# Kernel optimization log

Hardware: AMD Instinct MI355X
Metric: run time of the kernel (lower is better)

The kernel has to match this reference:

```python
import jax, jax.numpy as jnp
import numpy as np

EMBED = 1024
HEADS = 16
HEAD_DIM = EMBED // HEADS


def setup_inputs() -> dict:
    key = jax.random.key(0)
    ks = jax.random.split(key, 8)
    N, S = 4, 2048
    values = jax.random.normal(ks[0], (N, S, EMBED), dtype=jnp.float32)
    keys = jax.random.normal(ks[1], (N, S, EMBED), dtype=jnp.float32)
    query = jax.random.normal(ks[2], (N, S, EMBED), dtype=jnp.float32)
    mask = jnp.ones((N, 1, 1, S), dtype=jnp.int32)
    sd = 1.0 / np.sqrt(HEAD_DIM)
    Wv = jax.random.uniform(ks[3], (HEAD_DIM, HEAD_DIM), jnp.float32, -sd, sd)
    Wk = jax.random.uniform(ks[4], (HEAD_DIM, HEAD_DIM), jnp.float32, -sd, sd)
    Wq = jax.random.uniform(ks[5], (HEAD_DIM, HEAD_DIM), jnp.float32, -sd, sd)
    so = 1.0 / np.sqrt(EMBED)
    Wo = jax.random.uniform(ks[6], (EMBED, EMBED), jnp.float32, -so, so)
    bo = jax.random.uniform(ks[7], (EMBED,), jnp.float32, -so, so)
    return {"values": values, "keys": keys, "query": query, "mask": mask,
            "Wv": Wv, "Wk": Wk, "Wq": Wq, "Wo": Wo, "bo": bo}


def reference(values, keys, query, mask, Wv, Wk, Wq, Wo, bo):
    N, Sq, _ = query.shape
    # split heads: (N, L, H, D)
    v = values.reshape(N, -1, HEADS, HEAD_DIM)
    k = keys.reshape(N, -1, HEADS, HEAD_DIM)
    q = query.reshape(N, Sq, HEADS, HEAD_DIM)
    # per-head linear projections (torch Linear: x @ W.T)
    v = jnp.einsum('nlhd,ed->nlhe', v, Wv)
    k = jnp.einsum('nlhd,ed->nlhe', k, Wk)
    q = jnp.einsum('nqhd,ed->nqhe', q, Wq)
    # energy: (N, H, Q, K)
    energy = jnp.einsum('nqhd,nkhd->nhqk', q, k)
    energy = jnp.where(mask == 0, jnp.float32(-1e20), energy)
    # NOTE: original scales by sqrt(embed_size), not sqrt(head_dim)
    attention = jax.nn.softmax(energy / jnp.sqrt(jnp.float32(EMBED)), axis=3)
    out = jnp.einsum('nhql,nlhd->nqhd', attention, v).reshape(N, Sq, EMBED)
    return out @ Wo.T + bo
```

## Files before the change

### kernel.cpp

```cpp
#include <hip/hip_runtime.h>
#include <hip/hip_bf16.h>

typedef __bf16 bf16x8 __attribute__((ext_vector_type(8)));
typedef __bf16 bf16x4 __attribute__((ext_vector_type(4)));
typedef __bf16 bf16x2 __attribute__((ext_vector_type(2)));
typedef float  f32x4  __attribute__((ext_vector_type(4)));
typedef float  f32x16 __attribute__((ext_vector_type(16)));
typedef unsigned int u32;
typedef u32 u32x4 __attribute__((ext_vector_type(4)));

#define S_  2048
#define E_  1024
#define NH_ 64

__device__ __forceinline__ f32x4 mfma16(bf16x8 a, bf16x8 b, f32x4 c) {
    return __builtin_amdgcn_mfma_f32_16x16x32_bf16(a, b, c, 0, 0, 0);
}
__device__ __forceinline__ f32x16 mfma32(bf16x8 a, bf16x8 b, f32x16 c) {
    return __builtin_amdgcn_mfma_f32_32x32x16_bf16(a, b, c, 0, 0, 0);
}
__device__ __forceinline__ u32 pack2(float a, float b) {
    bf16x2 t; t[0] = (__bf16)a; t[1] = (__bf16)b;
    return __builtin_bit_cast(u32, t);
}
__device__ __forceinline__ void swap32(u32& a, u32& b) {
    asm("v_permlane32_swap_b32 %0, %1" : "+v"(a), "+v"(b));
}
__device__ __forceinline__ f32x16 zero16() {
    f32x16 z;
#pragma unroll
    for (int i = 0; i < 16; ++i) z[i] = 0.f;
    return z;
}
__device__ __forceinline__ void gload_lds16(const void* g, void* l) {
    __builtin_amdgcn_global_load_lds(
        (const __attribute__((address_space(1))) unsigned int*)g,
        (__attribute__((address_space(3))) unsigned int*)l, 16, 0, 0);
}

__global__ __launch_bounds__(256) void k_cast_wo(const float* __restrict__ Wo,
                                                 __bf16* __restrict__ Wob) {
    int i = (blockIdx.x * 256 + threadIdx.x) * 8;
    int o = i >> 10, e0 = i & 1023;
    float4 a = *(const float4*)(Wo + i);
    float4 b = *(const float4*)(Wo + i + 4);
    bf16x8 f;
    f[0] = (__bf16)a.x; f[1] = (__bf16)a.y; f[2] = (__bf16)a.z; f[3] = (__bf16)a.w;
    f[4] = (__bf16)b.x; f[5] = (__bf16)b.y; f[6] = (__bf16)b.z; f[7] = (__bf16)b.w;
    int e_swz = (e0 & ~63) | ((e0 & 63) ^ ((o & 7) << 3));
    *(bf16x8*)(Wob + (size_t)o * 1024 + e_swz) = f;
}

__global__ __launch_bounds__(256) void k_proj(const float* __restrict__ vin,
                                              const float* __restrict__ kin,
                                              const float* __restrict__ qin,
                                              const float* __restrict__ Wv,
                                              const float* __restrict__ Wk,
                                              const float* __restrict__ Wq,
                                              __bf16* __restrict__ Qws,
                                              __bf16* __restrict__ Kws,
                                              __bf16* __restrict__ Vt) {
    const int z = blockIdx.z;
    const float* in = (z == 0) ? vin : ((z == 1) ? kin : qin);
    const float* W  = (z == 0) ? Wv  : ((z == 1) ? Wk  : Wq);
    const float scale = (z == 2) ? 0.04508422f : 1.0f;
    const int bid  = blockIdx.x;
    const int nh   = bid >> 5;
    const int sblk = (bid & 31) << 6;
    const int n = nh >> 4, h = nh & 15;
    const int lane = threadIdx.x & 63, wid = threadIdx.x >> 6;
    const int l16 = lane & 15, g = lane >> 4;

    bf16x8 Bf[4][2];
#pragma unroll
    for (int nt = 0; nt < 4; ++nt)
#pragma unroll
        for (int ks = 0; ks < 2; ++ks) {
            const float* wp = W + (nt * 16 + l16) * 64 + ks * 32 + g * 8;
            float4 a = *(const float4*)wp;
            float4 b = *(const float4*)(wp + 4);
            bf16x8 f;
            f[0] = (__bf16)(a.x * scale); f[1] = (__bf16)(a.y * scale);
            f[2] = (__bf16)(a.z * scale); f[3] = (__bf16)(a.w * scale);
            f[4] = (__bf16)(b.x * scale); f[5] = (__bf16)(b.y * scale);
            f[6] = (__bf16)(b.z * scale); f[7] = (__bf16)(b.w * scale);
            Bf[nt][ks] = f;
        }

    const int s = sblk + wid * 16 + l16;
    const float* ip = in + ((size_t)n * S_ + s) * E_ + h * 64 + g * 8;
    bf16x8 Af[2];
#pragma unroll
    for (int ks = 0; ks < 2; ++ks) {
        float4 a = *(const float4*)(ip + ks * 32);
        float4 b = *(const float4*)(ip + ks * 32 + 4);
        bf16x8 f;
        f[0] = (__bf16)a.x; f[1] = (__bf16)a.y; f[2] = (__bf16)a.z; f[3] = (__bf16)a.w;
        f[4] = (__bf16)b.x; f[5] = (__bf16)b.y; f[6] = (__bf16)b.z; f[7] = (__bf16)b.w;
        Af[ks] = f;
    }

    f32x4 acc[4];
#pragma unroll
    for (int nt = 0; nt < 4; ++nt) { acc[nt][0] = 0.f; acc[nt][1] = 0.f; acc[nt][2] = 0.f; acc[nt][3] = 0.f; }

    if (z == 0) {
#pragma unroll
        for (int nt = 0; nt < 4; ++nt) {
            acc[nt] = mfma16(Bf[nt][0], Af[0], acc[nt]);
            acc[nt] = mfma16(Bf[nt][1], Af[1], acc[nt]);
        }
#pragma unroll
        for (int nt = 0; nt < 4; ++nt)
#pragma unroll
            for (int r = 0; r < 4; ++r) {
                int e = nt * 16 + g * 4 + r;
                int srow = sblk + wid * 16 + l16;
                int sc = srow ^ ((e & 7) << 3);
                Vt[((size_t)nh * 64 + e) * S_ + sc] = (__bf16)acc[nt][r];
            }
    } else {
#pragma unroll
        for (int nt = 0; nt < 4; ++nt) {
            acc[nt] = mfma16(Af[0], Bf[nt][0], acc[nt]);
            acc[nt] = mfma16(Af[1], Bf[nt][1], acc[nt]);
        }
        if (z == 1) {
#pragma unroll
            for (int nt = 0; nt < 4; ++nt)
#pragma unroll
                for (int r = 0; r < 4; ++r) {
                    int srow = sblk + wid * 16 + g * 4 + r;
                    int ec = (nt * 16 + l16) ^ ((srow & 7) << 3);
                    Kws[((size_t)nh * S_ + srow) * 64 + ec] = (__bf16)acc[nt][r];
                }
        } else {
#pragma unroll
            for (int nt = 0; nt < 4; ++nt)
#pragma unroll
                for (int r = 0; r < 4; ++r) {
                    int srow = sblk + wid * 16 + g * 4 + r;
                    Qws[((size_t)nh * S_ + srow) * 64 + nt * 16 + l16] = (__bf16)acc[nt][r];
                }
        }
    }
}

__global__ __launch_bounds__(256, 4) void k_attn(const __bf16* __restrict__ Qws,
                                                 const __bf16* __restrict__ Kws,
                                                 const __bf16* __restrict__ Vt,
                                                 const int* __restrict__ maskp,
                                                 __bf16* __restrict__ Xws) {
    __shared__ __align__(16) char lds[2][16384];
    const int tid = threadIdx.x, lane = tid & 63, wid = tid >> 6;
    const int l31 = lane & 31, hf = lane >> 5, h8 = hf * 8;
    const int v = blockIdx.x;
    const int u = v >> 3;
    const int nh = (v & 7) * 8 + (u & 7), qb = u >> 3;
    const int n = nh >> 4, hd = nh & 15;

    int az = 0;
    for (int i = tid; i < S_; i += 256) az |= (maskp[(size_t)n * S_ + i] == 0);
    const int anyzero = __syncthreads_or(az);

    const char* Kc = (const char*)(Kws + (size_t)nh * S_ * 64);
    const char* Vc = (const char*)(Vt  + (size_t)nh * 64 * S_);
    const __bf16* Qb = Qws + (size_t)nh * S_ * 64;

    const int q0 = qb * 128 + wid * 32;
    bf16x8 Qf[4];
#pragma unroll
    for (int dt = 0; dt < 4; ++dt)
        Qf[dt] = *(const bf16x8*)(Qb + (size_t)(q0 + l31) * 64 + dt * 16 + h8);

    f32x16 acc0 = zero16(), acc1 = zero16();
    float lsum = 0.f;

    auto stage = [&](int buf, int kb) {
        char* base = &lds[buf][0];
        const char* ks = Kc + (size_t)kb * 8192 + wid * 2048 + lane * 16;
        char* kd = base + wid * 2048;
        gload_lds16(ks, kd);
        gload_lds16(ks + 1024, kd + 1024);
        const int r0 = wid * 16 + (lane >> 3);
        const char* vs = Vc + (size_t)r0 * (S_ * 2) + (size_t)kb * 128 + (lane & 7) * 16;
        char* vd = base + 8192 + wid * 2048;
        gload_lds16(vs, vd);
        gload_lds16(vs + (size_t)8 * (S_ * 2), vd + 1024);
    };

    const int swz = (l31 & 7) << 4;

    stage(0, 0);
    int buf = 0;
    for (int kb = 0; kb < 32; ++kb) {
        __syncthreads();
        if (kb < 31) stage(buf ^ 1, kb + 1);
        char* base = &lds[buf][0];
        char* vbase = base + 8192;
        const int k0 = kb * 64;
#pragma unroll
        for (int kt = 0; kt < 2; ++kt) {
            bf16x8 K0 = *(const bf16x8*)(base + (kt * 32 + l31) * 128 + (((0 * 2 + hf) * 16) ^ swz));
            bf16x8 K1 = *(const bf16x8*)(base + (kt * 32 + l31) * 128 + (((1 * 2 + hf) * 16) ^ swz));
            bf16x8 K2 = *(const bf16x8*)(base + (kt * 32 + l31) * 128 + (((2 * 2 + hf) * 16) ^ swz));
            bf16x8 K3 = *(const bf16x8*)(base + (kt * 32 + l31) * 128 + (((3 * 2 + hf) * 16) ^ swz));
            __builtin_amdgcn_s_setprio(1);
            f32x16 s = zero16();
            s = mfma32(K0, Qf[0], s); s = mfma32(K1, Qf[1], s);
            s = mfma32(K2, Qf[2], s); s = mfma32(K3, Qf[3], s);
            __builtin_amdgcn_s_setprio(0);
            if (anyzero) {
#pragma unroll
                for (int r = 0; r < 16; ++r) {
                    int kk = k0 + kt * 32 + (r & 3) + 8 * (r >> 2) + 4 * hf;
                    if (maskp[(size_t)n * S_ + kk] == 0) s[r] = -1e30f;
                }
            }
            float p[16];
#pragma unroll
            for (int r = 0; r < 16; ++r) p[r] = __builtin_amdgcn_exp2f(s[r]);
            lsum += ((((p[0] + p[1]) + (p[2] + p[3])) + ((p[4] + p[5]) + (p[6] + p[7])))
                  + (((p[8] + p[9]) + (p[10] + p[11])) + ((p[12] + p[13]) + (p[14] + p[15]))));
            u32 w0 = pack2(p[0],  p[1]),  w1 = pack2(p[2],  p[3]);
            u32 w2 = pack2(p[4],  p[5]),  w3 = pack2(p[6],  p[7]);
            u32 w4 = pack2(p[8],  p[9]),  w5 = pack2(p[10], p[11]);
            u32 w6 = pack2(p[12], p[13]), w7 = pack2(p[14], p[15]);
            swap32(w0, w2); swap32(w1, w3); swap32(w4, w6); swap32(w5, w7);
            u32x4 t0; t0[0] = w0; t0[1] = w1; t0[2] = w2; t0[3] = w3;
            u32x4 t1; t1[0] = w4; t1[1] = w5; t1[2] = w6; t1[3] = w7;
            bf16x8 P0 = __builtin_bit_cast(bf16x8, t0);
            bf16x8 P1 = __builtin_bit_cast(bf16x8, t1);
            bf16x8 V00 = *(const bf16x8*)(vbase + (0 * 32 + l31) * 128 + ((((kt * 2 + 0) * 2 + hf) * 16) ^ swz));
            bf16x8 V01 = *(const bf16x8*)(vbase + (0 * 32 + l31) * 128 + ((((kt * 2 + 1) * 2 + hf) * 16) ^ swz));
            bf16x8 V10 = *(const bf16x8*)(vbase + (1 * 32 + l31) * 128 + ((((kt * 2 + 0) * 2 + hf) * 16) ^ swz));
            bf16x8 V11 = *(const bf16x8*)(vbase + (1 * 32 + l31) * 128 + ((((kt * 2 + 1) * 2 + hf) * 16) ^ swz));
            __builtin_amdgcn_s_setprio(1);
            acc0 = mfma32(V00, P0, acc0); acc0 = mfma32(V01, P1, acc0);
            acc1 = mfma32(V10, P0, acc1); acc1 = mfma32(V11, P1, acc1);
            __builtin_amdgcn_s_setprio(0);
        }
        buf ^= 1;
    }

    lsum += __shfl_xor(lsum, 32);
    const float inv = 1.0f / lsum;
    const int qg = q0 + l31;
    __bf16* Ob = Xws + ((size_t)(n * S_ + qg)) * E_ + hd * 64;
    const int qsw = (qg & 7) << 3;

    auto store_half = [&](const f32x16& a, int dv) {
#pragma unroll
        for (int rr = 0; rr < 4; ++rr) {
            bf16x4 o;
#pragma unroll
            for (int j = 0; j < 4; ++j) o[j] = (__bf16)(a[rr * 4 + j] * inv);
            int dsw = ((dv * 32 + rr * 8) ^ qsw) + hf * 4;
            *(bf16x4*)(Ob + dsw) = o;
        }
    };
    store_half(acc0, 0);
    store_half(acc1, 1);
}

__global__ __launch_bounds__(256) void k_out(const __bf16* __restrict__ Xws,
                                             const __bf16* __restrict__ Wob,
                                             const float* __restrict__ bo,
                                             float* __restrict__ out) {
    __shared__ __align__(16) char Al[2][16384];
    __shared__ __align__(16) char Bl[2][16384];
    const int tid = threadIdx.x, lane = tid & 63, wid = tid >> 6;
    const int l31 = lane & 31, hf = lane >> 5;
    const int v = blockIdx.x;
    const int id2 = (v & 7) * 64 + (v >> 3);
    const int mb = id2 >> 3, ob = id2 & 7;
    const int m0 = mb * 128, o0 = ob * 128;
    const int wr = wid >> 1, wc = wid & 1;

    const char* Xb = (const char*)Xws + (size_t)m0 * 2048;
    const char* Wb = (const char*)Wob + (size_t)o0 * 2048;
    const int r = tid >> 3, cb = (tid & 7) * 16;

    auto stage = [&](int buf, int kb) {
#pragma unroll
        for (int p = 0; p < 4; ++p) {
            gload_lds16(Xb + (size_t)(p * 32 + r) * 2048 + kb * 128 + cb,
                        &Al[buf][p * 4096 + wid * 1024]);
            gload_lds16(Wb + (size_t)(p * 32 + r) * 2048 + kb * 128 + cb,
                        &Bl[buf][p * 4096 + wid * 1024]);
        }
    };

    f32x16 acc00 = zero16(), acc01 = zero16(), acc10 = zero16(), acc11 = zero16();

    const int arow0 = (wr * 64 + l31) * 128;
    const int brow0 = (wc * 64 + l31) * 128;
    const int rsw = (l31 & 7) << 4;

    stage(0, 0);
    int buf = 0;
    for (int kb = 0; kb < 16; ++kb) {
        __syncthreads();
        if (kb < 15) stage(buf ^ 1, kb + 1);
        const char* ab = &Al[buf][0];
        const char* bb = &Bl[buf][0];
#pragma unroll
        for (int ks = 0; ks < 4; ++ks) {
            const int co = (ks * 32 + hf * 16) ^ rsw;
            bf16x8 A0 = *(const bf16x8*)(ab + arow0 + co);
            bf16x8 A1 = *(const bf16x8*)(ab + arow0 + 32 * 128 + co);
            bf16x8 B0 = *(const bf16x8*)(bb + brow0 + co);
            bf16x8 B1 = *(const bf16x8*)(bb + brow0 + 32 * 128 + co);
            __builtin_amdgcn_s_setprio(1);
            acc00 = mfma32(A0, B0, acc00);
            acc01 = mfma32(A0, B1, acc01);
            acc10 = mfma32(A1, B0, acc10);
            acc11 = mfma32(A1, B1, acc11);
            __builtin_amdgcn_s_setprio(0);
        }
        buf ^= 1;
    }

    const float bias0 = bo[o0 + wc * 64 + l31];
    const float bias1 = bo[o0 + wc * 64 + 32 + l31];
#pragma unroll
    for (int sm = 0; sm < 2; ++sm) {
        const f32x16& a0 = (sm == 0) ? acc00 : acc10;
        const f32x16& a1 = (sm == 0) ? acc01 : acc11;
#pragma unroll
        for (int rr = 0; rr < 4; ++rr)
#pragma unroll
            for (int j = 0; j < 4; ++j) {
                size_t m = (size_t)m0 + wr * 64 + sm * 32 + rr * 8 + hf * 4 + j;
                out[m * E_ + o0 + wc * 64 + l31]      = a0[rr * 4 + j] + bias0;
                out[m * E_ + o0 + wc * 64 + 32 + l31] = a1[rr * 4 + j] + bias1;
            }
    }
}

extern "C" void kernel_launch(void* const* d_in, const int* in_sizes, int n_in,
                              void* d_out, int out_size, void* d_ws, size_t ws_size,
                              hipStream_t stream) {
    const float* vin  = (const float*)d_in[0];
    const float* kin  = (const float*)d_in[1];
    const float* qin  = (const float*)d_in[2];
    const int*   mask = (const int*)d_in[3];
    const float* Wv   = (const float*)d_in[4];
    const float* Wk   = (const float*)d_in[5];
    const float* Wq   = (const float*)d_in[6];
    const float* Wo   = (const float*)d_in[7];
    const float* bo   = (const float*)d_in[8];

    __bf16* Qws = (__bf16*)d_ws;
    __bf16* Kws = Qws + (size_t)NH_ * S_ * 64;
    __bf16* Vt  = Kws + (size_t)NH_ * S_ * 64;
    __bf16* Xws = Vt  + (size_t)NH_ * S_ * 64;
    __bf16* Wob = Xws + (size_t)4 * S_ * E_;
    float* out = (float*)d_out;

    hipLaunchKernelGGL(k_cast_wo, dim3(512), dim3(256), 0, stream, Wo, Wob);
    hipLaunchKernelGGL(k_proj, dim3(2048, 1, 3), dim3(256), 0, stream,
                       vin, kin, qin, Wv, Wk, Wq, Qws, Kws, Vt);
    hipLaunchKernelGGL(k_attn, dim3(1024), dim3(256), 0, stream, Qws, Kws, Vt, mask, Xws);
    hipLaunchKernelGGL(k_out, dim3(512), dim3(256), 0, stream, Xws, Wob, bo, out);
}
```

Measured before the change: 170.2 us.

## Process two query tiles per wave in attention, sharing K/V fragments

Each attention wave now handles 64 query rows as two 32-row tiles that reuse the same K and V LDS fragments. This halves the grid, and launch bounds drop to 2 blocks per SIMD to make room for the extra registers. The LDS swizzle for K and V gains an extra 8-byte XOR bit, with matching changes in the projection writes, and fragments are read as two 8-byte loads, presumably to cut bank conflicts. The aim is to roughly halve LDS reads per MFMA. The cost is more register pressure, fewer resident blocks and more, narrower LDS load instructions.

```diff
diff --git a/kernel.cpp b/kernel.cpp
--- a/kernel.cpp
+++ b/kernel.cpp
@@ -36,6 +36,14 @@
     __builtin_amdgcn_global_load_lds(
         (const __attribute__((address_space(1))) unsigned int*)g,
         (__attribute__((address_space(3))) unsigned int*)l, 16, 0, 0);
+}
+__device__ __forceinline__ bf16x8 lds_frag(const char* p0, const char* p1) {
+    bf16x4 lo = *(const bf16x4*)p0;
+    bf16x4 hi = *(const bf16x4*)p1;
+    bf16x8 f;
+    f[0] = lo[0]; f[1] = lo[1]; f[2] = lo[2]; f[3] = lo[3];
+    f[4] = hi[0]; f[5] = hi[1]; f[6] = hi[2]; f[7] = hi[3];
+    return f;
 }
 
 __global__ __launch_bounds__(256) void k_cast_wo(const float* __restrict__ Wo,
@@ -116,7 +124,7 @@
             for (int r = 0; r < 4; ++r) {
                 int e = nt * 16 + g * 4 + r;
                 int srow = sblk + wid * 16 + l16;
-                int sc = srow ^ ((e & 7) << 3);
+                int sc = srow ^ (((e & 7) << 3) | (((e >> 3) & 1) << 2));
                 Vt[((size_t)nh * 64 + e) * S_ + sc] = (__bf16)acc[nt][r];
             }
     } else {
@@ -131,7 +139,7 @@
 #pragma unroll
                 for (int r = 0; r < 4; ++r) {
                     int srow = sblk + wid * 16 + g * 4 + r;
-                    int ec = (nt * 16 + l16) ^ ((srow & 7) << 3);
+                    int ec = (nt * 16 + l16) ^ (((srow & 7) << 3) | (((srow >> 3) & 1) << 2));
                     Kws[((size_t)nh * S_ + srow) * 64 + ec] = (__bf16)acc[nt][r];
                 }
         } else {
@@ -146,7 +154,7 @@
     }
 }
 
-__global__ __launch_bounds__(256, 4) void k_attn(const __bf16* __restrict__ Qws,
+__global__ __launch_bounds__(256, 2) void k_attn(const __bf16* __restrict__ Qws,
                                                  const __bf16* __restrict__ Kws,
                                                  const __bf16* __restrict__ Vt,
                                                  const int* __restrict__ maskp,
@@ -167,14 +175,16 @@
     const char* Vc = (const char*)(Vt  + (size_t)nh * 64 * S_);
     const __bf16* Qb = Qws + (size_t)nh * S_ * 64;
 
-    const int q0 = qb * 128 + wid * 32;
-    bf16x8 Qf[4];
-#pragma unroll
-    for (int dt = 0; dt < 4; ++dt)
-        Qf[dt] = *(const bf16x8*)(Qb + (size_t)(q0 + l31) * 64 + dt * 16 + h8);
-
-    f32x16 acc0 = zero16(), acc1 = zero16();
-    float lsum = 0.f;
+    const int q0 = qb * 256 + wid * 64;
+    bf16x8 QfA[4], QfB[4];
+#pragma unroll
+    for (int dt = 0; dt < 4; ++dt) {
+        QfA[dt] = *(const bf16x8*)(Qb + (size_t)(q0 + l31) * 64 + dt * 16 + h8);
+        QfB[dt] = *(const bf16x8*)(Qb + (size_t)(q0 + 32 + l31) * 64 + dt * 16 + h8);
+    }
+
+    f32x16 accA0 = zero16(), accA1 = zero16(), accB0 = zero16(), accB1 = zero16();
+    float lsumA = 0.f, lsumB = 0.f;
 
     auto stage = [&](int buf, int kb) {
         char* base = &lds[buf][0];
@@ -189,7 +199,32 @@
         gload_lds16(vs + (size_t)8 * (S_ * 2), vd + 1024);
     };
 
-    const int swz = (l31 & 7) << 4;
+    const int fs = ((l31 & 7) << 4) | (((l31 >> 3) & 1) << 3);
+
+    auto softmax = [&](const f32x16& s, float& ls, int kbase, bf16x8& P0, bf16x8& P1) {
+        f32x16 sv = s;
+        if (anyzero) {
+#pragma unroll
+            for (int r = 0; r < 16; ++r) {
+                int kk = kbase + (r & 3) + 8 * (r >> 2) + 4 * hf;
+                if (maskp[(size_t)n * S_ + kk] == 0) sv[r] = -1e30f;
+            }
+        }
+        float p[16];
+#pragma unroll
+        for (int r = 0; r < 16; ++r) p[r] = __builtin_amdgcn_exp2f(sv[r]);
+        ls += ((((p[0] + p[1]) + (p[2] + p[3])) + ((p[4] + p[5]) + (p[6] + p[7])))
+            + (((p[8] + p[9]) + (p[10] + p[11])) + ((p[12] + p[13]) + (p[14] + p[15]))));
+        u32 w0 = pack2(p[0],  p[1]),  w1 = pack2(p[2],  p[3]);
+        u32 w2 = pack2(p[4],  p[5]),  w3 = pack2(p[6],  p[7]);
+        u32 w4 = pack2(p[8],  p[9]),  w5 = pack2(p[10], p[11]);
+        u32 w6 = pack2(p[12], p[13]), w7 = pack2(p[14], p[15]);
+        swap32(w0, w2); swap32(w1, w3); swap32(w4, w6); swap32(w5, w7);
+        u32x4 t0; t0[0] = w0; t0[1] = w1; t0[2] = w2; t0[3] = w3;
+        u32x4 t1; t1[0] = w4; t1[1] = w5; t1[2] = w6; t1[3] = w7;
+        P0 = __builtin_bit_cast(bf16x8, t0);
+        P1 = __builtin_bit_cast(bf16x8, t1);
+    };
 
     stage(0, 0);
     int buf = 0;
@@ -201,66 +236,61 @@
         const int k0 = kb * 64;
 #pragma unroll
         for (int kt = 0; kt < 2; ++kt) {
-            bf16x8 K0 = *(const bf16x8*)(base + (kt * 32 + l31) * 128 + (((0 * 2 + hf) * 16) ^ swz));
-            bf16x8 K1 = *(const bf16x8*)(base + (kt * 32 + l31) * 128 + (((1 * 2 + hf) * 16) ^ swz));
-            bf16x8 K2 = *(const bf16x8*)(base + (kt * 32 + l31) * 128 + (((2 * 2 + hf) * 16) ^ swz));
-            bf16x8 K3 = *(const bf16x8*)(base + (kt * 32 + l31) * 128 + (((3 * 2 + hf) * 16) ^ swz));
+            const char* krow = base + (kt * 32 + l31) * 128;
+            bf16x8 K0 = lds_frag(krow + ((0 * 32 + hf * 16) ^ fs), krow + ((0 * 32 + hf * 16 + 8) ^ fs));
+            bf16x8 K1 = lds_frag(krow + ((1 * 32 + hf * 16) ^ fs), krow + ((1 * 32 + hf * 16 + 8) ^ fs));
+            bf16x8 K2 = lds_frag(krow + ((2 * 32 + hf * 16) ^ fs), krow + ((2 * 32 + hf * 16 + 8) ^ fs));
+            bf16x8 K3 = lds_frag(krow + ((3 * 32 + hf * 16) ^ fs), krow + ((3 * 32 + hf * 16 + 8) ^ fs));
             __builtin_amdgcn_s_setprio(1);
-            f32x16 s = zero16();
-            s = mfma32(K0, Qf[0], s); s = mfma32(K1, Qf[1], s);
-            s = mfma32(K2, Qf[2], s); s = mfma32(K3, Qf[3], s);
+            f32x16 sA = zero16(), sB = zero16();
+            sA = mfma32(K0, QfA[0], sA); sA = mfma32(K1, QfA[1], sA);
+            sA = mfma32(K2, QfA[2], sA); sA = mfma32(K3, QfA[3], sA);
+            sB = mfma32(K0, QfB[0], sB); sB = mfma32(K1, QfB[1], sB);
+            sB = mfma32(K2, QfB[2], sB); sB = mfma32(K3, QfB[3], sB);
             __builtin_amdgcn_s_setprio(0);
-            if (anyzero) {
-#pragma unroll
-                for (int r = 0; r < 16; ++r) {
-                    int kk = k0 + kt * 32 + (r & 3) + 8 * (r >> 2) + 4 * hf;
-                    if (maskp[(size_t)n * S_ + kk] == 0) s[r] = -1e30f;
-                }
+            const char* v0row = vbase + (0 * 32 + l31) * 128;
+            const char* v1row = vbase + (1 * 32 + l31) * 128;
+            const int o0b = (kt * 2 + 0) * 32 + hf * 16;
+            const int o1b = (kt * 2 + 1) * 32 + hf * 16;
+            bf16x8 V00 = lds_frag(v0row + (o0b ^ fs), v0row + ((o0b + 8) ^ fs));
+            bf16x8 V01 = lds_frag(v0row + (o1b ^ fs), v0row + ((o1b + 8) ^ fs));
+            bf16x8 V10 = lds_frag(v1row + (o0b ^ fs), v1row + ((o0b + 8) ^ fs));
+            bf16x8 V11 = lds_frag(v1row + (o1b ^ fs), v1row + ((o1b + 8) ^ fs));
+            bf16x8 PA0, PA1, PB0, PB1;
+            softmax(sA, lsumA, k0 + kt * 32, PA0, PA1);
+            softmax(sB, lsumB, k0 + kt * 32, PB0, PB1);
+            __builtin_amdgcn_s_setprio(1);
+            accA0 = mfma32(V00, PA0, accA0); accA0 = mfma32(V01, PA1, accA0);
+            accA1 = mfma32(V10, PA0, accA1); accA1 = mfma32(V11, PA1, accA1);
+            accB0 = mfma32(V00, PB0, accB0); accB0 = mfma32(V01, PB1, accB0);
+            accB1 = mfma32(V10, PB0, accB1); accB1 = mfma32(V11, PB1, accB1);
+            __builtin_amdgcn_s_setprio(0);
+        }
+        buf ^= 1;
+    }
+
+    lsumA += __shfl_xor(lsumA, 32);
+    lsumB += __shfl_xor(lsumB, 32);
+    const float invA = 1.0f / lsumA, invB = 1.0f / lsumB;
+
+    auto store_q = [&](const f32x16& a0, const f32x16& a1, int qg, float inv) {
+        __bf16* Ob = Xws + ((size_t)(n * S_ + qg)) * E_ + hd * 64;
+        const int qsw = (qg & 7) << 3;
+#pragma unroll
+        for (int dv = 0; dv < 2; ++dv) {
+            const f32x16& a = dv ? a1 : a0;
+#pragma unroll
+            for (int rr = 0; rr < 4; ++rr) {
+                bf16x4 o;
+#pragma unroll
+                for (int j = 0; j < 4; ++j) o[j] = (__bf16)(a[rr * 4 + j] * inv);
+                int dsw = ((dv * 32 + rr * 8) ^ qsw) + hf * 4;
+                *(bf16x4*)(Ob + dsw) = o;
             }
-            float p[16];
-#pragma unroll
-            for (int r = 0; r < 16; ++r) p[r] = __builtin_amdgcn_exp2f(s[r]);
-            lsum += ((((p[0] + p[1]) + (p[2] + p[3])) + ((p[4] + p[5]) + (p[6] + p[7])))
-                  + (((p[8] + p[9]) + (p[10] + p[11])) + ((p[12] + p[13]) + (p[14] + p[15]))));
-            u32 w0 = pack2(p[0],  p[1]),  w1 = pack2(p[2],  p[3]);
-            u32 w2 = pack2(p[4],  p[5]),  w3 = pack2(p[6],  p[7]);
-            u32 w4 = pack2(p[8],  p[9]),  w5 = pack2(p[10], p[11]);
-            u32 w6 = pack2(p[12], p[13]), w7 = pack2(p[14], p[15]);
-            swap32(w0, w2); swap32(w1, w3); swap32(w4, w6); swap32(w5, w7);
-            u32x4 t0; t0[0] = w0; t0[1] = w1; t0[2] = w2; t0[3] = w3;
-            u32x4 t1; t1[0] = w4; t1[1] = w5; t1[2] = w6; t1[3] = w7;
-            bf16x8 P0 = __builtin_bit_cast(bf16x8, t0);
-            bf16x8 P1 = __builtin_bit_cast(bf16x8, t1);
-            bf16x8 V00 = *(const bf16x8*)(vbase + (0 * 32 + l31) * 128 + ((((kt * 2 + 0) * 2 + hf) * 16) ^ swz));
-            bf16x8 V01 = *(const bf16x8*)(vbase + (0 * 32 + l31) * 128 + ((((kt * 2 + 1) * 2 + hf) * 16) ^ swz));
-            bf16x8 V10 = *(const bf16x8*)(vbase + (1 * 32 + l31) * 128 + ((((kt * 2 + 0) * 2 + hf) * 16) ^ swz));
-            bf16x8 V11 = *(const bf16x8*)(vbase + (1 * 32 + l31) * 128 + ((((kt * 2 + 1) * 2 + hf) * 16) ^ swz));
-            __builtin_amdgcn_s_setprio(1);
-            acc0 = mfma32(V00, P0, acc0); acc0 = mfma32(V01, P1, acc0);
-            acc1 = mfma32(V10, P0, acc1); acc1 = mfma32(V11, P1, acc1);
-            __builtin_amdgcn_s_setprio(0);
-        }
-        buf ^= 1;
-    }
-
-    lsum += __shfl_xor(lsum, 32);
-    const float inv = 1.0f / lsum;
-    const int qg = q0 + l31;
-    __bf16* Ob = Xws + ((size_t)(n * S_ + qg)) * E_ + hd * 64;
-    const int qsw = (qg & 7) << 3;
-
-    auto store_half = [&](const f32x16& a, int dv) {
-#pragma unroll
-        for (int rr = 0; rr < 4; ++rr) {
-            bf16x4 o;
-#pragma unroll
-            for (int j = 0; j < 4; ++j) o[j] = (__bf16)(a[rr * 4 + j] * inv);
-            int dsw = ((dv * 32 + rr * 8) ^ qsw) + hf * 4;
-            *(bf16x4*)(Ob + dsw) = o;
         }
     };
-    store_half(acc0, 0);
-    store_half(acc1, 1);
+    store_q(accA0, accA1, q0 + l31, invA);
+    store_q(accB0, accB1, q0 + 32 + l31, invB);
 }
 
 __global__ __launch_bounds__(256) void k_out(const __bf16* __restrict__ Xws,
@@ -361,6 +391,6 @@
     hipLaunchKernelGGL(k_cast_wo, dim3(512), dim3(256), 0, stream, Wo, Wob);
     hipLaunchKernelGGL(k_proj, dim3(2048, 1, 3), dim3(256), 0, stream,
                        vin, kin, qin, Wv, Wk, Wq, Qws, Kws, Vt);
-    hipLaunchKernelGGL(k_attn, dim3(1024), dim3(256), 0, stream, Qws, Kws, Vt, mask, Xws);
+    hipLaunchKernelGGL(k_attn, dim3(512), dim3(256), 0, stream, Qws, Kws, Vt, mask, Xws);
     hipLaunchKernelGGL(k_out, dim3(512), dim3(256), 0, stream, Xws, Wob, bo, out);
 }
```

Result: faster. 166.8 us (-2.0%).

## Stage projection outputs through LDS and refine K/V swizzle with split 8-byte reads

Applied to the files above, without the earlier changes.

The projection kernel now writes its MFMA results into a padded LDS tile and then emits coalesced 16-byte rows to the Q, K and V^T workspaces, replacing scattered 2-byte global stores. The K/V swizzle gains an extra bit at 8-byte granularity, and the attention kernel reads each fragment as two 8-byte LDS loads to match, aiming to reduce bank conflicts. The softmax code is moved into a lambda and the V loads are issued before it so their latency can overlap with the exp work. This costs twice as many LDS read instructions in the attention inner loop, plus an extra barrier and LDS use in the projection kernel.

```diff
diff --git a/kernel.cpp b/kernel.cpp
--- a/kernel.cpp
+++ b/kernel.cpp
@@ -7,6 +7,7 @@
 typedef float  f32x4  __attribute__((ext_vector_type(4)));
 typedef float  f32x16 __attribute__((ext_vector_type(16)));
 typedef unsigned int u32;
+typedef u32 u32x2 __attribute__((ext_vector_type(2)));
 typedef u32 u32x4 __attribute__((ext_vector_type(4)));
 
 #define S_  2048
@@ -36,6 +37,12 @@
     __builtin_amdgcn_global_load_lds(
         (const __attribute__((address_space(1))) unsigned int*)g,
         (__attribute__((address_space(3))) unsigned int*)l, 16, 0, 0);
+}
+__device__ __forceinline__ bf16x8 lds_frag(const char* p0, const char* p1) {
+    u32x2 lo = *(const u32x2*)p0;
+    u32x2 hi = *(const u32x2*)p1;
+    u32x4 t; t[0] = lo[0]; t[1] = lo[1]; t[2] = hi[0]; t[3] = hi[1];
+    return __builtin_bit_cast(bf16x8, t);
 }
 
 __global__ __launch_bounds__(256) void k_cast_wo(const float* __restrict__ Wo,
@@ -51,6 +58,7 @@
     *(bf16x8*)(Wob + (size_t)o * 1024 + e_swz) = f;
 }
 
+#define TP 72
 __global__ __launch_bounds__(256) void k_proj(const float* __restrict__ vin,
                                               const float* __restrict__ kin,
                                               const float* __restrict__ qin,
@@ -60,6 +68,7 @@
                                               __bf16* __restrict__ Qws,
                                               __bf16* __restrict__ Kws,
                                               __bf16* __restrict__ Vt) {
+    __shared__ __align__(16) __bf16 tile[64 * TP];
     const int z = blockIdx.z;
     const float* in = (z == 0) ? vin : ((z == 1) ? kin : qin);
     const float* W  = (z == 0) ? Wv  : ((z == 1) ? Wk  : Wq);
@@ -107,43 +116,46 @@
     if (z == 0) {
 #pragma unroll
         for (int nt = 0; nt < 4; ++nt) {
+            acc[nt] = mfma16(Af[0], Bf[nt][0], acc[nt]);
+            acc[nt] = mfma16(Af[1], Bf[nt][1], acc[nt]);
+        }
+#pragma unroll
+        for (int nt = 0; nt < 4; ++nt) {
+            int d = nt * 16 + l16;
+            int scol = (wid * 16 + g * 4) ^ (((d & 7) << 3) | (((d >> 3) & 1) << 2));
+            bf16x4 o;
+#pragma unroll
+            for (int r = 0; r < 4; ++r) o[r] = (__bf16)acc[nt][r];
+            *(bf16x4*)(tile + d * TP + scol) = o;
+        }
+    } else {
+#pragma unroll
+        for (int nt = 0; nt < 4; ++nt) {
             acc[nt] = mfma16(Bf[nt][0], Af[0], acc[nt]);
             acc[nt] = mfma16(Bf[nt][1], Af[1], acc[nt]);
         }
-#pragma unroll
-        for (int nt = 0; nt < 4; ++nt)
-#pragma unroll
-            for (int r = 0; r < 4; ++r) {
-                int e = nt * 16 + g * 4 + r;
-                int srow = sblk + wid * 16 + l16;
-                int sc = srow ^ ((e & 7) << 3);
-                Vt[((size_t)nh * 64 + e) * S_ + sc] = (__bf16)acc[nt][r];
-            }
-    } else {
+        const int sl = wid * 16 + l16;
+        const int fk = (z == 1) ? (((sl & 7) << 3) | (((sl >> 3) & 1) << 2)) : 0;
 #pragma unroll
         for (int nt = 0; nt < 4; ++nt) {
-            acc[nt] = mfma16(Af[0], Bf[nt][0], acc[nt]);
-            acc[nt] = mfma16(Af[1], Bf[nt][1], acc[nt]);
-        }
-        if (z == 1) {
-#pragma unroll
-            for (int nt = 0; nt < 4; ++nt)
-#pragma unroll
-                for (int r = 0; r < 4; ++r) {
-                    int srow = sblk + wid * 16 + g * 4 + r;
-                    int ec = (nt * 16 + l16) ^ ((srow & 7) << 3);
-                    Kws[((size_t)nh * S_ + srow) * 64 + ec] = (__bf16)acc[nt][r];
-                }
-        } else {
-#pragma unroll
-            for (int nt = 0; nt < 4; ++nt)
-#pragma unroll
-                for (int r = 0; r < 4; ++r) {
-                    int srow = sblk + wid * 16 + g * 4 + r;
-                    Qws[((size_t)nh * S_ + srow) * 64 + nt * 16 + l16] = (__bf16)acc[nt][r];
-                }
-        }
-    }
+            int e0 = (nt * 16 + g * 4) ^ fk;
+            bf16x4 o;
+#pragma unroll
+            for (int r = 0; r < 4; ++r) o[r] = (__bf16)acc[nt][r];
+            *(bf16x4*)(tile + sl * TP + e0) = o;
+        }
+    }
+    __syncthreads();
+
+    const int trow = threadIdx.x >> 2, tc = (threadIdx.x & 3) * 16;
+    bf16x8 v0 = *(const bf16x8*)(tile + trow * TP + tc);
+    bf16x8 v1 = *(const bf16x8*)(tile + trow * TP + tc + 8);
+    __bf16* dst;
+    if (z == 0)      dst = Vt  + ((size_t)nh * 64 + trow) * S_ + sblk + tc;
+    else if (z == 1) dst = Kws + ((size_t)nh * S_ + sblk + trow) * 64 + tc;
+    else             dst = Qws + ((size_t)nh * S_ + sblk + trow) * 64 + tc;
+    *(bf16x8*)dst = v0;
+    *(bf16x8*)(dst + 8) = v1;
 }
 
 __global__ __launch_bounds__(256, 4) void k_attn(const __bf16* __restrict__ Qws,
@@ -189,7 +201,32 @@
         gload_lds16(vs + (size_t)8 * (S_ * 2), vd + 1024);
     };
 
-    const int swz = (l31 & 7) << 4;
+    const int fs = ((l31 & 7) << 4) | (((l31 >> 3) & 1) << 3);
+
+    auto softmax = [&](const f32x16& s, float& ls, int kbase, bf16x8& P0, bf16x8& P1) {
+        f32x16 sv = s;
+        if (anyzero) {
+#pragma unroll
+            for (int r = 0; r < 16; ++r) {
+                int kk = kbase + (r & 3) + 8 * (r >> 2) + 4 * hf;
+                if (maskp[(size_t)n * S_ + kk] == 0) sv[r] = -1e30f;
+            }
+        }
+        float p[16];
+#pragma unroll
+        for (int r = 0; r < 16; ++r) p[r] = __builtin_amdgcn_exp2f(sv[r]);
+        ls += ((((p[0] + p[1]) + (p[2] + p[3])) + ((p[4] + p[5]) + (p[6] + p[7])))
+            + (((p[8] + p[9]) + (p[10] + p[11])) + ((p[12] + p[13]) + (p[14] + p[15]))));
+        u32 w0 = pack2(p[0],  p[1]),  w1 = pack2(p[2],  p[3]);
+        u32 w2 = pack2(p[4],  p[5]),  w3 = pack2(p[6],  p[7]);
+        u32 w4 = pack2(p[8],  p[9]),  w5 = pack2(p[10], p[11]);
+        u32 w6 = pack2(p[12], p[13]), w7 = pack2(p[14], p[15]);
+        swap32(w0, w2); swap32(w1, w3); swap32(w4, w6); swap32(w5, w7);
+        u32x4 t0; t0[0] = w0; t0[1] = w1; t0[2] = w2; t0[3] = w3;
+        u32x4 t1; t1[0] = w4; t1[1] = w5; t1[2] = w6; t1[3] = w7;
+        P0 = __builtin_bit_cast(bf16x8, t0);
+        P1 = __builtin_bit_cast(bf16x8, t1);
+    };
 
     stage(0, 0);
     int buf = 0;
@@ -201,40 +238,26 @@
         const int k0 = kb * 64;
 #pragma unroll
         for (int kt = 0; kt < 2; ++kt) {
-            bf16x8 K0 = *(const bf16x8*)(base + (kt * 32 + l31) * 128 + (((0 * 2 + hf) * 16) ^ swz));
-            bf16x8 K1 = *(const bf16x8*)(base + (kt * 32 + l31) * 128 + (((1 * 2 + hf) * 16) ^ swz));
-            bf16x8 K2 = *(const bf16x8*)(base + (kt * 32 + l31) * 128 + (((2 * 2 + hf) * 16) ^ swz));
-            bf16x8 K3 = *(const bf16x8*)(base + (kt * 32 + l31) * 128 + (((3 * 2 + hf) * 16) ^ swz));
+            const char* krow = base + (kt * 32 + l31) * 128;
+            bf16x8 K0 = lds_frag(krow + ((0 * 32 + hf * 16) ^ fs), krow + ((0 * 32 + hf * 16 + 8) ^ fs));
+            bf16x8 K1 = lds_frag(krow + ((1 * 32 + hf * 16) ^ fs), krow + ((1 * 32 + hf * 16 + 8) ^ fs));
+            bf16x8 K2 = lds_frag(krow + ((2 * 32 + hf * 16) ^ fs), krow + ((2 * 32 + hf * 16 + 8) ^ fs));
+            bf16x8 K3 = lds_frag(krow + ((3 * 32 + hf * 16) ^ fs), krow + ((3 * 32 + hf * 16 + 8) ^ fs));
             __builtin_amdgcn_s_setprio(1);
-            f32x16 s = zero16();
-            s = mfma32(K0, Qf[0], s); s = mfma32(K1, Qf[1], s);
-            s = mfma32(K2, Qf[2], s); s = mfma32(K3, Qf[3], s);
+            f32x16 sA = zero16();
+            sA = mfma32(K0, Qf[0], sA); sA = mfma32(K1, Qf[1], sA);
+            sA = mfma32(K2, Qf[2], sA); sA = mfma32(K3, Qf[3], sA);
             __builtin_amdgcn_s_setprio(0);
-            if (anyzero) {
-#pragma unroll
-                for (int r = 0; r < 16; ++r) {
-                    int kk = k0 + kt * 32 + (r & 3) + 8 * (r >> 2) + 4 * hf;
-                    if (maskp[(size_t)n * S_ + kk] == 0) s[r] = -1e30f;
-                }
-            }
-            float p[16];
-#pragma unroll
-            for (int r = 0; r < 16; ++r) p[r] = __builtin_amdgcn_exp2f(s[r]);
-            lsum += ((((p[0] + p[1]) + (p[2] + p[3])) + ((p[4] + p[5]) + (p[6] + p[7])))
-                  + (((p[8] + p[9]) + (p[10] + p[11])) + ((p[12] + p[13]) + (p[14] + p[15]))));
-            u32 w0 = pack2(p[0],  p[1]),  w1 = pack2(p[2],  p[3]);
-            u32 w2 = pack2(p[4],  p[5]),  w3 = pack2(p[6],  p[7]);
-            u32 w4 = pack2(p[8],  p[9]),  w5 = pack2(p[10], p[11]);
-            u32 w6 = pack2(p[12], p[13]), w7 = pack2(p[14], p[15]);
-            swap32(w0, w2); swap32(w1, w3); swap32(w4, w6); swap32(w5, w7);
-            u32x4 t0; t0[0] = w0; t0[1] = w1; t0[2] = w2; t0[3] = w3;
-            u32x4 t1; t1[0] = w4; t1[1] = w5; t1[2] = w6; t1[3] = w7;
-            bf16x8 P0 = __builtin_bit_cast(bf16x8, t0);
-            bf16x8 P1 = __builtin_bit_cast(bf16x8, t1);
-            bf16x8 V00 = *(const bf16x8*)(vbase + (0 * 32 + l31) * 128 + ((((kt * 2 + 0) * 2 + hf) * 16) ^ swz));
-            bf16x8 V01 = *(const bf16x8*)(vbase + (0 * 32 + l31) * 128 + ((((kt * 2 + 1) * 2 + hf) * 16) ^ swz));
-            bf16x8 V10 = *(const bf16x8*)(vbase + (1 * 32 + l31) * 128 + ((((kt * 2 + 0) * 2 + hf) * 16) ^ swz));
-            bf16x8 V11 = *(const bf16x8*)(vbase + (1 * 32 + l31) * 128 + ((((kt * 2 + 1) * 2 + hf) * 16) ^ swz));
+            const char* v0row = vbase + (0 * 32 + l31) * 128;
+            const char* v1row = vbase + (1 * 32 + l31) * 128;
+            const int o0b = (kt * 2 + 0) * 32 + hf * 16;
+            const int o1b = (kt * 2 + 1) * 32 + hf * 16;
+            bf16x8 V00 = lds_frag(v0row + (o0b ^ fs), v0row + ((o0b + 8) ^ fs));
+            bf16x8 V01 = lds_frag(v0row + (o1b ^ fs), v0row + ((o1b + 8) ^ fs));
+            bf16x8 V10 = lds_frag(v1row + (o0b ^ fs), v1row + ((o0b + 8) ^ fs));
+            bf16x8 V11 = lds_frag(v1row + (o1b ^ fs), v1row + ((o1b + 8) ^ fs));
+            bf16x8 P0, P1;
+            softmax(sA, lsum, k0 + kt * 32, P0, P1);
             __builtin_amdgcn_s_setprio(1);
             acc0 = mfma32(V00, P0, acc0); acc0 = mfma32(V01, P1, acc0);
             acc1 = mfma32(V10, P0, acc1); acc1 = mfma32(V11, P1, acc1);
```

After: 178.0 us. 1.05x slower.
